# Optimization experiments

Hardware: AMD Instinct MI355X
Metric: run time of the kernel (lower is better)

## Reference

```python
import jax, jax.numpy as jnp
import numpy as np

DIM = 384
NUM_HEADS = 12
HEAD_DIM = DIM // NUM_HEADS
SCALE = HEAD_DIM ** -0.5


def setup_inputs() -> dict:
    key = jax.random.key(0)
    k_x, k_w, k_o = jax.random.split(key, 3)
    B, n, N, C = 2, 64, 256, DIM
    x = jax.random.normal(k_x, (B, n, N, C), dtype=jnp.float32)
    # kaiming_uniform_(a=sqrt(5)) on a (3C, C) matrix -> bound = 1/sqrt(C)
    bound = 1.0 / np.sqrt(C)
    in_proj_weight = jax.random.uniform(k_w, (3 * C, C), dtype=jnp.float32, minval=-bound, maxval=bound)
    in_proj_bias = jnp.zeros((3 * C,), dtype=jnp.float32)
    ob = 1.0 / np.sqrt(C)
    out_proj_weight = jax.random.uniform(k_o, (C, C), dtype=jnp.float32, minval=-ob, maxval=ob)
    return {"x": x, "in_proj_weight": in_proj_weight, "in_proj_bias": in_proj_bias,
            "out_proj_weight": out_proj_weight}


def reference(x, in_proj_weight, in_proj_bias, out_proj_weight):
    B, n, N, C = x.shape
    H, d = NUM_HEADS, C // NUM_HEADS
    # fused QKV projection: F.linear(x, W, b) = x @ W.T + b
    qkv = jnp.einsum('bwnc,oc->bwno', x, in_proj_weight) + in_proj_bias
    q, k, v = jnp.split(qkv, 3, axis=-1)                      # each [B, n, N, C]
    # [B, n, N, C] -> [B, n, H, N, d]
    def heads(t):
        return t.reshape(B, n, N, H, d).transpose(0, 1, 3, 2, 4)
    q = heads(q) * SCALE
    k = heads(k)
    v = heads(v)
    attn = jax.nn.softmax(jnp.einsum('bwhqd,bwhkd->bwhqk', q, k), axis=-1)
    out = jnp.einsum('bwhqk,bwhkd->bwhqd', attn, v)           # [B, n, H, N, d]
    out = out.transpose(0, 1, 3, 2, 4).reshape(B, n, N, C)
    out = jnp.einsum('bwnc,oc->bwno', out, out_proj_weight)   # out_proj has no bias
    return out
```

## Files before the change

kernel.cpp:

```cpp
#include <hip/hip_runtime.h>
#include <hip/hip_bf16.h>

typedef __attribute__((ext_vector_type(4)))  float  f32x4;
typedef __attribute__((ext_vector_type(16))) float  f32x16;
typedef __attribute__((ext_vector_type(8)))  short  bf16x8;
typedef __attribute__((ext_vector_type(8)))  ushort u16x8;

#define C_DIM   384
#define QKV_DIM 1152
#define NHEAD   12
#define HDIM    32
#define NTOK    256

__device__ __forceinline__ ushort f2bf(float f) {
    union { __hip_bfloat16 h; ushort u; } cv;
    cv.h = __float2bfloat16(f);
    return cv.u;
}

__global__ void cvt_kernel(const float* __restrict__ in, ushort* __restrict__ out, int n4) {
    int i = blockIdx.x * blockDim.x + threadIdx.x;
    if (i >= n4) return;
    const float4 v = reinterpret_cast<const float4*>(in)[i];
    ushort4 o;
    o.x = f2bf(v.x); o.y = f2bf(v.y); o.z = f2bf(v.z); o.w = f2bf(v.w);
    reinterpret_cast<ushort4*>(out)[i] = o;
}

template<int BIAS, int OUTF32, int AHB, int OHB>
__global__ __launch_bounds__(256) void gemm_bt(const ushort* __restrict__ A,
                                               const ushort* __restrict__ Bw,
                                               const float* __restrict__ bias,
                                               void* __restrict__ Cout,
                                               int M, int N, int K) {
    __shared__ __align__(16) ushort As[128 * 64];
    __shared__ __align__(16) ushort Bs[128 * 64];

    const int t    = threadIdx.x;
    const int lane = t & 63;
    const int wave = t >> 6;
    const int wr   = (wave >> 1) * 64;
    const int wc   = (wave & 1) * 64;
    const int lr   = lane & 15;
    const int lg   = lane >> 4;

    const int gx  = gridDim.x;
    const int nwg = gx * gridDim.y;
    const int h   = blockIdx.y * gx + blockIdx.x;
    const int cpx = nwg >> 3;
    const int lin = (h & 7) * cpx + (h >> 3);
    const int by  = lin / gx;
    const int bx  = lin - by * gx;
    const int mBase = by * 128;
    const int nBase = bx * 128;

    f32x4 acc[4][4] = {};
    const int nK = K >> 6;

    for (int kt = 0; kt < nK; ++kt) {
        const int k0 = kt << 6;
#pragma unroll
        for (int it = 0; it < 4; ++it) {
            const int idx = it * 256 + t;
            const int r   = idx >> 3;
            const int cb  = (idx & 7) ^ (r & 7);
            const ushort* ga;
            if (AHB) {
                const int k = k0 + cb * 8;
                ga = A + ((size_t)(k >> 5) * M + (mBase + r)) * 32 + (k & 31);
            } else {
                ga = A + (size_t)(mBase + r) * K + k0 + cb * 8;
            }
            __builtin_amdgcn_global_load_lds(
                (const __attribute__((address_space(1))) void*)ga,
                (__attribute__((address_space(3))) void*)(&As[it * 2048 + wave * 512]),
                16, 0, 0);
            const ushort* gb = Bw + (size_t)(nBase + r) * K + k0 + cb * 8;
            __builtin_amdgcn_global_load_lds(
                (const __attribute__((address_space(1))) void*)gb,
                (__attribute__((address_space(3))) void*)(&Bs[it * 2048 + wave * 512]),
                16, 0, 0);
        }
        __syncthreads();

#pragma unroll
        for (int kk = 0; kk < 2; ++kk) {
            bf16x8 af[4], bfr[4];
#pragma unroll
            for (int m = 0; m < 4; ++m) {
                const int r = wr + m * 16 + lr;
                af[m] = *reinterpret_cast<const bf16x8*>(
                    &As[r * 64 + (((kk * 4 + lg) ^ (r & 7)) << 3)]);
            }
#pragma unroll
            for (int n = 0; n < 4; ++n) {
                const int r = wc + n * 16 + lr;
                bfr[n] = *reinterpret_cast<const bf16x8*>(
                    &Bs[r * 64 + (((kk * 4 + lg) ^ (r & 7)) << 3)]);
            }
#pragma unroll
            for (int m = 0; m < 4; ++m)
#pragma unroll
                for (int n = 0; n < 4; ++n)
                    acc[m][n] = __builtin_amdgcn_mfma_f32_16x16x32_bf16(af[m], bfr[n], acc[m][n], 0, 0, 0);
        }
        __syncthreads();
    }

#pragma unroll
    for (int n = 0; n < 4; ++n) {
        const int col = nBase + wc + n * 16 + lr;
        const float bv = BIAS ? bias[col] : 0.f;
        const int sel  = OHB ? (col / 384) : 0;
        const int c384 = OHB ? (col - sel * 384) : 0;
#pragma unroll
        for (int m = 0; m < 4; ++m) {
            const int row0 = mBase + wr + m * 16 + lg * 4;
#pragma unroll
            for (int j = 0; j < 4; ++j) {
                const float v = acc[m][n][j] + bv;
                const int row = row0 + j;
                if (OUTF32) {
                    reinterpret_cast<float*>(Cout)[(size_t)row * N + col] = v;
                } else if (OHB) {
                    reinterpret_cast<ushort*>(Cout)[
                        ((size_t)(sel * NHEAD + (c384 >> 5)) * M + row) * 32 + (c384 & 31)] = f2bf(v);
                } else {
                    reinterpret_cast<ushort*>(Cout)[(size_t)row * N + col] = f2bf(v);
                }
            }
        }
    }
}

__global__ __launch_bounds__(256) void attn_kernel(const ushort* __restrict__ qkv,
                                                   ushort* __restrict__ att,
                                                   int Mtok) {
    __shared__ __align__(16) ushort Ks[NTOK * HDIM];
    __shared__ __align__(16) ushort Vt[HDIM * NTOK];

    const int bid = blockIdx.x;
    const int win = bid / NHEAD;
    const int h   = bid % NHEAD;

    const int t    = threadIdx.x;
    const int lane = t & 63;
    const int wave = t >> 6;
    const int l31  = lane & 31;
    const int h5   = lane >> 5;

    const size_t winRow = (size_t)win * NTOK;
    const ushort* Qbase = qkv + ((size_t)h * Mtok + winRow) * HDIM;
    const ushort* Kbase = qkv + ((size_t)(NHEAD + h) * Mtok + winRow) * HDIM;
    const ushort* Vbase = qkv + ((size_t)(2 * NHEAD + h) * Mtok + winRow) * HDIM;

#pragma unroll
    for (int it = 0; it < 4; ++it) {
        const int idx = it * 256 + t;
        const int key = idx >> 2;
        const int cb  = (idx & 3) ^ (key & 3);
        const ushort* gk = Kbase + key * HDIM + cb * 8;
        __builtin_amdgcn_global_load_lds(
            (const __attribute__((address_space(1))) void*)gk,
            (__attribute__((address_space(3))) void*)(&Ks[it * 2048 + wave * 512]),
            16, 0, 0);
    }
#pragma unroll
    for (int it = 0; it < 4; ++it) {
        const int idx = it * 256 + t;
        const int key = idx >> 2;
        const int cb  = idx & 3;
        u16x8 v8 = *reinterpret_cast<const u16x8*>(Vbase + key * HDIM + cb * 8);
#pragma unroll
        for (int jj = 0; jj < 8; ++jj) {
            const int dd  = cb * 8 + jj;
            const int blk = (key >> 3) ^ (dd & 7) ^ ((2 * (dd >> 3)) & 6);
            Vt[dd * NTOK + blk * 8 + (key & 7)] = v8[jj];
        }
    }
    __syncthreads();

    const float c1   = 0.25503509f;
    const int   vmsk = (l31 & 7) ^ ((2 * (l31 >> 3)) & 6);
    const int   kmsk = l31 & 3;
    const int   q0   = wave * 64;

#pragma unroll 1
    for (int ch = 0; ch < 2; ++ch) {
        const int qrow = q0 + ch * 32 + l31;
        const bf16x8 qf0 = *reinterpret_cast<const bf16x8*>(
            Qbase + (size_t)qrow * HDIM + h5 * 8);
        const bf16x8 qf1 = *reinterpret_cast<const bf16x8*>(
            Qbase + (size_t)qrow * HDIM + 16 + h5 * 8);

        float sm0 = 0.f, sm1 = 0.f, sm2 = 0.f, sm3 = 0.f;
#pragma unroll
        for (int tt = 0; tt < 8; ++tt) {
            const int key = tt * 32 + l31;
            const bf16x8 kf0 = *reinterpret_cast<const bf16x8*>(
                &Ks[key * HDIM + ((h5 ^ kmsk) << 3)]);
            const bf16x8 kf1 = *reinterpret_cast<const bf16x8*>(
                &Ks[key * HDIM + (((2 + h5) ^ kmsk) << 3)]);
            f32x16 s = {};
            s = __builtin_amdgcn_mfma_f32_32x32x16_bf16(kf0, qf0, s, 0, 0, 0);
            s = __builtin_amdgcn_mfma_f32_32x32x16_bf16(kf1, qf1, s, 0, 0, 0);
#pragma unroll
            for (int r = 0; r < 16; r += 4) {
                sm0 += __builtin_amdgcn_exp2f(s[r + 0] * c1);
                sm1 += __builtin_amdgcn_exp2f(s[r + 1] * c1);
                sm2 += __builtin_amdgcn_exp2f(s[r + 2] * c1);
                sm3 += __builtin_amdgcn_exp2f(s[r + 3] * c1);
            }
        }
        float sm = (sm0 + sm1) + (sm2 + sm3);
        sm += __shfl_xor(sm, 32, 64);
        const float inv = __builtin_amdgcn_rcpf(sm);

        f32x16 O = {};
#pragma unroll
        for (int tt = 0; tt < 8; ++tt) {
            const int key = tt * 32 + l31;
            const bf16x8 kf0 = *reinterpret_cast<const bf16x8*>(
                &Ks[key * HDIM + ((h5 ^ kmsk) << 3)]);
            const bf16x8 kf1 = *reinterpret_cast<const bf16x8*>(
                &Ks[key * HDIM + (((2 + h5) ^ kmsk) << 3)]);
            f32x16 s = {};
            s = __builtin_amdgcn_mfma_f32_32x32x16_bf16(kf0, qf0, s, 0, 0, 0);
            s = __builtin_amdgcn_mfma_f32_32x32x16_bf16(kf1, qf1, s, 0, 0, 0);

            uint pk8[8];
#pragma unroll
            for (int m = 0; m < 8; ++m) {
                const int r = 4 * (m >> 1) + 2 * (m & 1);
                const float lo = __builtin_amdgcn_exp2f(s[r + 0] * c1) * inv;
                const float hi = __builtin_amdgcn_exp2f(s[r + 1] * c1) * inv;
                uint d;
                asm("v_cvt_pk_bf16_f32 %0, %1, %2" : "=v"(d) : "v"(lo), "v"(hi));
                pk8[m] = d;
            }

#pragma unroll
            for (int k16 = 0; k16 < 2; ++k16) {
                const int mb = 4 * k16;
                const uint s0 = h5 ? pk8[mb + 0] : pk8[mb + 2];
                const uint s1 = h5 ? pk8[mb + 1] : pk8[mb + 3];
                const uint x0 = (uint)__shfl_xor((int)s0, 32, 64);
                const uint x1 = (uint)__shfl_xor((int)s1, 32, 64);
                union { uint u[4]; bf16x8 v; } pw;
                pw.u[0] = h5 ? x0 : pk8[mb + 0];
                pw.u[1] = h5 ? x1 : pk8[mb + 1];
                pw.u[2] = h5 ? pk8[mb + 2] : x0;
                pw.u[3] = h5 ? pk8[mb + 3] : x1;
                const int blk = (4 * tt + 2 * k16 + h5) ^ vmsk;
                const bf16x8 vf = *reinterpret_cast<const bf16x8*>(
                    &Vt[l31 * NTOK + blk * 8]);
                O = __builtin_amdgcn_mfma_f32_32x32x16_bf16(pw.v, vf, O, 0, 0, 0);
            }
        }

        ushort* obase = att + ((size_t)h * Mtok + winRow + q0 + ch * 32) * HDIM + l31;
#pragma unroll
        for (int r = 0; r < 16; ++r) {
            const int qr = (r & 3) + 8 * (r >> 2) + 4 * h5;
            obase[(size_t)qr * HDIM] = f2bf(O[r]);
        }
    }
}

extern "C" void kernel_launch(void* const* d_in, const int* in_sizes, int n_in,
                              void* d_out, int out_size, void* d_ws, size_t ws_size,
                              hipStream_t stream) {
    const float* x     = (const float*)d_in[0];
    const float* w_in  = (const float*)d_in[1];
    const float* b_in  = (const float*)d_in[2];
    const float* w_out = (const float*)d_in[3];

    const int M    = in_sizes[0] / C_DIM;
    const int nWin = M / NTOK;

    char* ws = (char*)d_ws;
    size_t off = 0;
    ushort* xb    = (ushort*)(ws + off); off += (size_t)M * C_DIM * 2;
    ushort* qkvb  = (ushort*)(ws + off); off += (size_t)M * QKV_DIM * 2;
    ushort* attb  = (ushort*)(ws + off); off += (size_t)M * C_DIM * 2;
    ushort* wqkvb = (ushort*)(ws + off); off += (size_t)QKV_DIM * C_DIM * 2;
    ushort* woutb = (ushort*)(ws + off);

    cvt_kernel<<<(M * C_DIM / 4 + 255) / 256, 256, 0, stream>>>(x, xb, M * C_DIM / 4);
    cvt_kernel<<<(QKV_DIM * C_DIM / 4 + 255) / 256, 256, 0, stream>>>(w_in, wqkvb, QKV_DIM * C_DIM / 4);
    cvt_kernel<<<(C_DIM * C_DIM / 4 + 255) / 256, 256, 0, stream>>>(w_out, woutb, C_DIM * C_DIM / 4);

    gemm_bt<1, 0, 0, 1><<<dim3(QKV_DIM / 128, M / 128), 256, 0, stream>>>(
        xb, wqkvb, b_in, qkvb, M, QKV_DIM, C_DIM);

    attn_kernel<<<nWin * NHEAD, 256, 0, stream>>>(qkvb, attb, M);

    gemm_bt<0, 1, 1, 0><<<dim3(C_DIM / 128, M / 128), 256, 0, stream>>>(
        attb, woutb, nullptr, d_out, M, C_DIM, C_DIM);
}
```

Baseline: 129.2 us.

## Double-buffer GEMM LDS tiles and shrink N tile to 64

```diff
diff --git a/kernel.cpp b/kernel.cpp
--- a/kernel.cpp
+++ b/kernel.cpp
@@ -28,36 +28,36 @@
 }
 
 template<int BIAS, int OUTF32, int AHB, int OHB>
-__global__ __launch_bounds__(256) void gemm_bt(const ushort* __restrict__ A,
-                                               const ushort* __restrict__ Bw,
-                                               const float* __restrict__ bias,
-                                               void* __restrict__ Cout,
-                                               int M, int N, int K) {
-    __shared__ __align__(16) ushort As[128 * 64];
-    __shared__ __align__(16) ushort Bs[128 * 64];
+__global__ __launch_bounds__(256, 3) void gemm_bt(const ushort* __restrict__ A,
+                                                  const ushort* __restrict__ Bw,
+                                                  const float* __restrict__ bias,
+                                                  void* __restrict__ Cout,
+                                                  int M, int N, int K) {
+    __shared__ __align__(16) ushort As[2][128 * 64];
+    __shared__ __align__(16) ushort Bs[2][64 * 64];
 
     const int t    = threadIdx.x;
     const int lane = t & 63;
     const int wave = t >> 6;
     const int wr   = (wave >> 1) * 64;
-    const int wc   = (wave & 1) * 64;
+    const int wc   = (wave & 1) * 32;
     const int lr   = lane & 15;
     const int lg   = lane >> 4;
 
     const int gx  = gridDim.x;
     const int nwg = gx * gridDim.y;
-    const int h   = blockIdx.y * gx + blockIdx.x;
+    const int hw  = blockIdx.y * gx + blockIdx.x;
     const int cpx = nwg >> 3;
-    const int lin = (h & 7) * cpx + (h >> 3);
+    const int lin = (hw & 7) * cpx + (hw >> 3);
     const int by  = lin / gx;
     const int bx  = lin - by * gx;
     const int mBase = by * 128;
-    const int nBase = bx * 128;
-
-    f32x4 acc[4][4] = {};
+    const int nBase = bx * 64;
+
+    f32x4 acc[4][2] = {};
     const int nK = K >> 6;
 
-    for (int kt = 0; kt < nK; ++kt) {
+    auto stage = [&](int kt, int c) {
         const int k0 = kt << 6;
 #pragma unroll
         for (int it = 0; it < 4; ++it) {
@@ -73,42 +73,59 @@
             }
             __builtin_amdgcn_global_load_lds(
                 (const __attribute__((address_space(1))) void*)ga,
-                (__attribute__((address_space(3))) void*)(&As[it * 2048 + wave * 512]),
+                (__attribute__((address_space(3))) void*)(&As[c][it * 2048 + wave * 512]),
                 16, 0, 0);
+        }
+#pragma unroll
+        for (int it = 0; it < 2; ++it) {
+            const int idx = it * 256 + t;
+            const int r   = idx >> 3;
+            const int cb  = (idx & 7) ^ (r & 7);
             const ushort* gb = Bw + (size_t)(nBase + r) * K + k0 + cb * 8;
             __builtin_amdgcn_global_load_lds(
                 (const __attribute__((address_space(1))) void*)gb,
-                (__attribute__((address_space(3))) void*)(&Bs[it * 2048 + wave * 512]),
+                (__attribute__((address_space(3))) void*)(&Bs[c][it * 2048 + wave * 512]),
                 16, 0, 0);
         }
-        __syncthreads();
+    };
+
+    stage(0, 0);
+    __syncthreads();
+    int cur = 0;
+
+    for (int kt = 0; kt < nK; ++kt) {
+        if (kt + 1 < nK) stage(kt + 1, cur ^ 1);
 
 #pragma unroll
         for (int kk = 0; kk < 2; ++kk) {
-            bf16x8 af[4], bfr[4];
+            bf16x8 af[4], bfr[2];
 #pragma unroll
             for (int m = 0; m < 4; ++m) {
                 const int r = wr + m * 16 + lr;
                 af[m] = *reinterpret_cast<const bf16x8*>(
-                    &As[r * 64 + (((kk * 4 + lg) ^ (r & 7)) << 3)]);
-            }
-#pragma unroll
-            for (int n = 0; n < 4; ++n) {
+                    &As[cur][r * 64 + (((kk * 4 + lg) ^ (r & 7)) << 3)]);
+            }
+#pragma unroll
+            for (int n = 0; n < 2; ++n) {
                 const int r = wc + n * 16 + lr;
                 bfr[n] = *reinterpret_cast<const bf16x8*>(
-                    &Bs[r * 64 + (((kk * 4 + lg) ^ (r & 7)) << 3)]);
+                    &Bs[cur][r * 64 + (((kk * 4 + lg) ^ (r & 7)) << 3)]);
             }
 #pragma unroll
             for (int m = 0; m < 4; ++m)
 #pragma unroll
-                for (int n = 0; n < 4; ++n)
+                for (int n = 0; n < 2; ++n)
                     acc[m][n] = __builtin_amdgcn_mfma_f32_16x16x32_bf16(af[m], bfr[n], acc[m][n], 0, 0, 0);
         }
-        __syncthreads();
-    }
-
-#pragma unroll
-    for (int n = 0; n < 4; ++n) {
+
+        if (kt + 1 < nK) {
+            __syncthreads();
+            cur ^= 1;
+        }
+    }
+
+#pragma unroll
+    for (int n = 0; n < 2; ++n) {
         const int col = nBase + wc + n * 16 + lr;
         const float bv = BIAS ? bias[col] : 0.f;
         const int sel  = OHB ? (col / 384) : 0;
@@ -290,11 +307,11 @@
     cvt_kernel<<<(QKV_DIM * C_DIM / 4 + 255) / 256, 256, 0, stream>>>(w_in, wqkvb, QKV_DIM * C_DIM / 4);
     cvt_kernel<<<(C_DIM * C_DIM / 4 + 255) / 256, 256, 0, stream>>>(w_out, woutb, C_DIM * C_DIM / 4);
 
-    gemm_bt<1, 0, 0, 1><<<dim3(QKV_DIM / 128, M / 128), 256, 0, stream>>>(
+    gemm_bt<1, 0, 0, 1><<<dim3(QKV_DIM / 64, M / 128), 256, 0, stream>>>(
         xb, wqkvb, b_in, qkvb, M, QKV_DIM, C_DIM);
 
     attn_kernel<<<nWin * NHEAD, 256, 0, stream>>>(qkvb, attb, M);
 
-    gemm_bt<0, 1, 1, 0><<<dim3(C_DIM / 128, M / 128), 256, 0, stream>>>(
+    gemm_bt<0, 1, 1, 0><<<dim3(C_DIM / 64, M / 128), 256, 0, stream>>>(
         attb, woutb, nullptr, d_out, M, C_DIM, C_DIM);
 }
```

After: 129.3 us. About the same (+0.1%).
